# Kernel optimization log

Measured on AMD Instinct MI355X. Metric: run time of the kernel, lower is better.

The kernel has to match this reference:

```python
import jax, jax.numpy as jnp
import numpy as np

# LIF neuron constants (the CUDA kernel source is not shipped; these are the
# standard fused SNN semantics documented for this layer)
V_DECAY = 0.9       # membrane leak per step
V_THRESH = 1.0      # spike threshold
REFRAC_PERIOD = 5.0 # refractory timer reset value (in steps)

B_SZ, SEQ, HID, STATE = 8, 4096, 1024, 64


def setup_inputs() -> dict:
    key = jax.random.key(0)
    k1, k2, k3, k4, k5 = jax.random.split(key, 5)
    return {
        "input": jax.random.normal(k1, (B_SZ, SEQ, HID), dtype=jnp.float32),
        "ssm_A": jax.random.normal(k2, (STATE, STATE), dtype=jnp.float32) * 0.01,
        "ssm_B": jax.random.normal(k3, (STATE, 1), dtype=jnp.float32) * 0.1,
        "ssm_C": jax.random.normal(k4, (1, STATE), dtype=jnp.float32) * 0.1,
        "ssm_D": jax.random.normal(k5, (1, 1), dtype=jnp.float32) * 0.01,
    }


def reference(input, ssm_A, ssm_B, ssm_C, ssm_D):
    batch, seq_len, hidden = input.shape
    state = ssm_A.shape[0]

    # initial states (module.forward always starts from zeros)
    v0 = jnp.zeros((batch, hidden), dtype=jnp.float32)
    r0 = jnp.zeros((batch, hidden), dtype=jnp.float32)
    h0 = jnp.zeros((batch, state), dtype=jnp.float32)

    Bvec = ssm_B[:, 0]      # [state]
    Cvec = ssm_C[0, :]      # [state]
    Dsc = ssm_D[0, 0]       # scalar

    def step(carry, x_t):
        v, r, h = carry
        # --- SNN membrane + refractory update ---
        v = v * V_DECAY + x_t
        active = r <= 0.0
        spike = jnp.where(active & (v >= V_THRESH), 1.0, 0.0)  # [B,H]
        v = jnp.where(spike > 0.0, 0.0, v)
        r = jnp.where(spike > 0.0, REFRAC_PERIOD, jnp.maximum(r - 1.0, 0.0))
        # --- SSM recurrence, driven by pooled spike rate (scalar per batch) ---
        u = jnp.mean(spike, axis=-1)                 # [B]
        h = jnp.einsum('ns,bs->bn', ssm_A, h) + u[:, None] * Bvec  # [B,N]
        y = h @ Cvec + Dsc * u                       # [B]
        out_t = spike + y[:, None]                   # [B,H]
        return (v, r, h), out_t

    xs = jnp.swapaxes(input, 0, 1)                   # [S,B,H]
    _, ys = jax.lax.scan(step, (v0, r0, h0), xs)
    return jnp.swapaxes(ys, 0, 1)                    # [B,S,H]
```

## Files before the change

### kernel.cpp

```cpp
#include <hip/hip_runtime.h>
#include <cstdint>
#include <cstddef>

#define B_SZ   8
#define SEQ    4096
#define HID    1024
#define NCH    8
#define CHUNK  512
#define WARM   256
#define JTAP   16
#define TS     32

typedef float vfloat4 __attribute__((ext_vector_type(4)));

__device__ __forceinline__ void snn_step(float& v, float& r, float xv, bool& s) {
  v = __fadd_rn(__fmul_rn(v, 0.9f), xv);
  s = (r <= 0.0f) && (v >= 1.0f);
  v = s ? 0.0f : v;
  r = s ? 5.0f : fmaxf(r - 1.0f, 0.0f);
}

__device__ __forceinline__ void proc32_emit(const float* xv, float& v, float& r, int lane,
                                            unsigned long long* __restrict__ sp, int t) {
  unsigned long long my = 0;
  #pragma unroll
  for (int k = 0; k < 32; ++k) {
    bool s; snn_step(v, r, xv[k], s);
    unsigned long long m = __ballot(s);
    my = ((lane & 31) == k) ? m : my;
  }
  if (lane < 32) sp[t + lane] = my;
}

__device__ __forceinline__ void proc32_warm(const float* xv, float& v, float& r) {
  #pragma unroll
  for (int k = 0; k < 32; ++k) { bool s; snn_step(v, r, xv[k], s); }
}

__global__ __launch_bounds__(256) void snn_kernel(const float* __restrict__ x,
                                                  unsigned long long* __restrict__ spk) {
  const int hid  = blockIdx.x * 256 + threadIdx.x;
  const int b    = blockIdx.y;
  const int c    = blockIdx.z;
  const int lane = threadIdx.x & 63;
  const int wv   = hid >> 6;
  const int t0   = c * CHUNK;
  const int t1   = t0 + CHUNK;
  const int tw   = (t0 >= WARM) ? (t0 - WARM) : 0;
  const float* __restrict__ xp = x + (size_t)(b * SEQ) * HID + hid;
  unsigned long long* __restrict__ sp = spk + (size_t)(b * 16 + wv) * SEQ;

  float v = 0.0f, r = 0.0f;
  float xa[32], xb[32];

  #pragma unroll
  for (int k = 0; k < 32; ++k) xa[k] = xp[(size_t)(tw + k) * HID];

  for (int t = tw; t < t1; t += 64) {
    #pragma unroll
    for (int k = 0; k < 32; ++k) xb[k] = xp[(size_t)(t + 32 + k) * HID];

    if (t >= t0) proc32_emit(xa, v, r, lane, sp, t);
    else         proc32_warm(xa, v, r);

    if (t + 64 < t1) {
      #pragma unroll
      for (int k = 0; k < 32; ++k) xa[k] = xp[(size_t)(t + 64 + k) * HID];
    }

    if (t + 32 >= t0) proc32_emit(xb, v, r, lane, sp, t + 32);
    else              proc32_warm(xb, v, r);
  }
}

__global__ __launch_bounds__(256) void yout_kernel(const unsigned long long* __restrict__ spk,
                                                   const float* __restrict__ A,
                                                   const float* __restrict__ Bv,
                                                   const float* __restrict__ Cv,
                                                   const float* __restrict__ Dp,
                                                   vfloat4* __restrict__ out) {
  __shared__ unsigned long long lm[16][TS + JTAP];
  __shared__ float ws[JTAP];
  __shared__ float su[TS + JTAP];
  __shared__ float sy[TS];

  const int tid = threadIdx.x;
  const int b   = blockIdx.y;
  const int t0  = blockIdx.x * TS;
  const unsigned long long* __restrict__ sb = spk + (size_t)b * 16 * SEQ;

  if (tid < 64) {
    const int lane = tid;
    float arow[64];
    #pragma unroll 8
    for (int s2 = 0; s2 < 64; ++s2) arow[s2] = A[lane * 64 + s2];
    float p = Bv[lane];
    const float cv = Cv[lane];
    for (int m = 0; m < JTAP; ++m) {
      float t = cv * p;
      #pragma unroll
      for (int off = 32; off; off >>= 1) t += __shfl_xor(t, off);
      if (lane == 0) ws[m] = t;
      float n0 = 0.f, n1 = 0.f, n2 = 0.f, n3 = 0.f;
      #pragma unroll
      for (int s2 = 0; s2 < 64; s2 += 4) {
        n0 = fmaf(arow[s2 + 0], __shfl(p, s2 + 0), n0);
        n1 = fmaf(arow[s2 + 1], __shfl(p, s2 + 1), n1);
        n2 = fmaf(arow[s2 + 2], __shfl(p, s2 + 2), n2);
        n3 = fmaf(arow[s2 + 3], __shfl(p, s2 + 3), n3);
      }
      p = (n0 + n1) + (n2 + n3);
    }
  } else {
    const int i = tid - 64;
    if (i < TS + JTAP) {
      const int t = t0 - JTAP + i;
      #pragma unroll
      for (int wv = 0; wv < 16; ++wv)
        lm[wv][i] = (t >= 0) ? sb[(size_t)wv * SEQ + t] : 0ull;
    }
  }
  __syncthreads();

  if (tid < TS + JTAP) {
    int cc = 0;
    #pragma unroll
    for (int wv = 0; wv < 16; ++wv) cc += __popcll(lm[wv][tid]);
    su[tid] = cc * (1.0f / 1024.0f);
  }
  __syncthreads();

  if (tid < TS) {
    float acc = Dp[0] * su[JTAP + tid];
    #pragma unroll
    for (int m = 0; m < JTAP; ++m) acc = fmaf(ws[m], su[JTAP + tid - m], acc);
    sy[tid] = acc;
  }
  __syncthreads();

  const int wv = tid >> 4;
  const int sh = (tid & 15) * 4;
  vfloat4* op = out + (size_t)(b * SEQ + t0) * 256 + tid;
  #pragma unroll 8
  for (int j = 0; j < TS; ++j) {
    const unsigned long long m = lm[wv][JTAP + j];
    const float yv = sy[j];
    vfloat4 o;
    o.x = ((m >> (sh + 0)) & 1ull) ? 1.0f + yv : yv;
    o.y = ((m >> (sh + 1)) & 1ull) ? 1.0f + yv : yv;
    o.z = ((m >> (sh + 2)) & 1ull) ? 1.0f + yv : yv;
    o.w = ((m >> (sh + 3)) & 1ull) ? 1.0f + yv : yv;
    __builtin_nontemporal_store(o, &op[(size_t)j * 256]);
  }
}

extern "C" void kernel_launch(void* const* d_in, const int* in_sizes, int n_in,
                              void* d_out, int out_size, void* d_ws, size_t ws_size,
                              hipStream_t stream) {
  const float* x  = (const float*)d_in[0];
  const float* A  = (const float*)d_in[1];
  const float* Bv = (const float*)d_in[2];
  const float* Cv = (const float*)d_in[3];
  const float* Dp = (const float*)d_in[4];

  unsigned long long* spk = (unsigned long long*)d_ws;

  dim3 g1(HID / 256, B_SZ, NCH);
  snn_kernel<<<g1, 256, 0, stream>>>(x, spk);

  dim3 g2(SEQ / TS, B_SZ);
  yout_kernel<<<g2, 256, 0, stream>>>(spk, A, Bv, Cv, Dp, (vfloat4*)d_out);
}
```

Baseline: 284.1 us.

## Split y computation from output write and double SNN chunk parallelism

Halves the SNN chunk length (16 chunks of 256 steps with a 256-step warmup), doubling grid parallelism at the cost of more redundant warmup work. The combined y/output kernel is split in two. A new ssm_y kernel computes the pooled spike rate and the 16-tap y filter for 256 timesteps per block, so the 64-lane A-power setup is amortized over far more timesteps, and writes y to a workspace buffer. A separate out kernel then streams the output tiles with small 16-timestep blocks, adding one extra launch and a small y round trip through global memory.

```diff
diff --git a/kernel.cpp b/kernel.cpp
--- a/kernel.cpp
+++ b/kernel.cpp
@@ -5,11 +5,12 @@
 #define B_SZ   8
 #define SEQ    4096
 #define HID    1024
-#define NCH    8
-#define CHUNK  512
+#define NCH    16
+#define CHUNK  256
 #define WARM   256
 #define JTAP   16
-#define TS     32
+#define TS3    16
+#define YTS    256
 
 typedef float vfloat4 __attribute__((ext_vector_type(4)));
 
@@ -73,20 +74,18 @@
   }
 }
 
-__global__ __launch_bounds__(256) void yout_kernel(const unsigned long long* __restrict__ spk,
-                                                   const float* __restrict__ A,
-                                                   const float* __restrict__ Bv,
-                                                   const float* __restrict__ Cv,
-                                                   const float* __restrict__ Dp,
-                                                   vfloat4* __restrict__ out) {
-  __shared__ unsigned long long lm[16][TS + JTAP];
+__global__ __launch_bounds__(256) void ssm_y_kernel(const unsigned long long* __restrict__ spk,
+                                                    const float* __restrict__ A,
+                                                    const float* __restrict__ Bv,
+                                                    const float* __restrict__ Cv,
+                                                    const float* __restrict__ Dp,
+                                                    float* __restrict__ y) {
   __shared__ float ws[JTAP];
-  __shared__ float su[TS + JTAP];
-  __shared__ float sy[TS];
+  __shared__ float su[YTS + JTAP];
 
   const int tid = threadIdx.x;
   const int b   = blockIdx.y;
-  const int t0  = blockIdx.x * TS;
+  const int t0  = blockIdx.x * YTS;
   const unsigned long long* __restrict__ sb = spk + (size_t)b * 16 * SEQ;
 
   if (tid < 64) {
@@ -113,37 +112,47 @@
     }
   } else {
     const int i = tid - 64;
-    if (i < TS + JTAP) {
-      const int t = t0 - JTAP + i;
+    for (int j = i; j < YTS + JTAP; j += 192) {
+      const int t = t0 - JTAP + j;
+      int cc = 0;
       #pragma unroll
       for (int wv = 0; wv < 16; ++wv)
-        lm[wv][i] = (t >= 0) ? sb[(size_t)wv * SEQ + t] : 0ull;
+        cc += (t >= 0) ? __popcll(sb[(size_t)wv * SEQ + t]) : 0;
+      su[j] = cc * (1.0f / 1024.0f);
     }
   }
   __syncthreads();
 
-  if (tid < TS + JTAP) {
-    int cc = 0;
+  {
+    const int j = tid;
+    float acc = Dp[0] * su[JTAP + j];
     #pragma unroll
-    for (int wv = 0; wv < 16; ++wv) cc += __popcll(lm[wv][tid]);
-    su[tid] = cc * (1.0f / 1024.0f);
+    for (int m = 0; m < JTAP; ++m) acc = fmaf(ws[m], su[JTAP + j - m], acc);
+    y[(size_t)b * SEQ + t0 + j] = acc;
   }
-  __syncthreads();
+}
 
-  if (tid < TS) {
-    float acc = Dp[0] * su[JTAP + tid];
-    #pragma unroll
-    for (int m = 0; m < JTAP; ++m) acc = fmaf(ws[m], su[JTAP + tid - m], acc);
-    sy[tid] = acc;
-  }
+__global__ __launch_bounds__(256) void out_kernel(const unsigned long long* __restrict__ spk,
+                                                  const float* __restrict__ y,
+                                                  vfloat4* __restrict__ out) {
+  __shared__ unsigned long long lm[16][TS3 + 1];
+  __shared__ float sy[TS3];
+
+  const int tid = threadIdx.x;
+  const int b   = blockIdx.y;
+  const int t0  = blockIdx.x * TS3;
+  const unsigned long long* __restrict__ sb = spk + (size_t)b * 16 * SEQ;
+
+  lm[tid >> 4][tid & 15] = sb[(size_t)(tid >> 4) * SEQ + t0 + (tid & 15)];
+  if (tid < TS3) sy[tid] = y[(size_t)b * SEQ + t0 + tid];
   __syncthreads();
 
   const int wv = tid >> 4;
   const int sh = (tid & 15) * 4;
   vfloat4* op = out + (size_t)(b * SEQ + t0) * 256 + tid;
-  #pragma unroll 8
-  for (int j = 0; j < TS; ++j) {
-    const unsigned long long m = lm[wv][JTAP + j];
+  #pragma unroll
+  for (int j = 0; j < TS3; ++j) {
+    const unsigned long long m = lm[wv][j];
     const float yv = sy[j];
     vfloat4 o;
     o.x = ((m >> (sh + 0)) & 1ull) ? 1.0f + yv : yv;
@@ -164,10 +173,14 @@
   const float* Dp = (const float*)d_in[4];
 
   unsigned long long* spk = (unsigned long long*)d_ws;
+  float* yv = (float*)((char*)d_ws + ((size_t)B_SZ * 16 * SEQ * 8));
 
   dim3 g1(HID / 256, B_SZ, NCH);
   snn_kernel<<<g1, 256, 0, stream>>>(x, spk);
 
-  dim3 g2(SEQ / TS, B_SZ);
-  yout_kernel<<<g2, 256, 0, stream>>>(spk, A, Bv, Cv, Dp, (vfloat4*)d_out);
+  dim3 g2(SEQ / YTS, B_SZ);
+  ssm_y_kernel<<<g2, 256, 0, stream>>>(spk, A, Bv, Cv, Dp, yv);
+
+  dim3 g3(SEQ / TS3, B_SZ);
+  out_kernel<<<g3, 256, 0, stream>>>(spk, yv, (vfloat4*)d_out);
 }
```

Measured after the change: 287.1 us. No clear change (+1.1%).

## Fuse SNN scan and output kernels into one cooperative kernel with grid sync

Applied to the files above, without the earlier changes.

Merges the spike-generation kernel and the SSM/output kernel into a single cooperative launch of 256 blocks, separated by a grid-wide barrier, which removes one kernel launch and the gap between the two kernels. The output phase now handles 128 timesteps per block instead of 32, and the shared spike-mask tile is transposed and padded to spread the load work across threads. The nontemporal output store is replaced by a plain store. The costs are the grid-sync overhead and larger per-block output tiles, and the design relies on all 256 blocks being co-resident.

```diff
diff --git a/kernel.cpp b/kernel.cpp
--- a/kernel.cpp
+++ b/kernel.cpp
@@ -1,6 +1,9 @@
 #include <hip/hip_runtime.h>
+#include <hip/hip_cooperative_groups.h>
 #include <cstdint>
 #include <cstddef>
+
+namespace cg = cooperative_groups;
 
 #define B_SZ   8
 #define SEQ    4096
@@ -9,7 +12,7 @@
 #define CHUNK  512
 #define WARM   256
 #define JTAP   16
-#define TS     32
+#define YTS    128
 
 typedef float vfloat4 __attribute__((ext_vector_type(4)));
 
@@ -37,57 +40,64 @@
   for (int k = 0; k < 32; ++k) { bool s; snn_step(v, r, xv[k], s); }
 }
 
-__global__ __launch_bounds__(256) void snn_kernel(const float* __restrict__ x,
-                                                  unsigned long long* __restrict__ spk) {
-  const int hid  = blockIdx.x * 256 + threadIdx.x;
-  const int b    = blockIdx.y;
-  const int c    = blockIdx.z;
-  const int lane = threadIdx.x & 63;
-  const int wv   = hid >> 6;
-  const int t0   = c * CHUNK;
-  const int t1   = t0 + CHUNK;
-  const int tw   = (t0 >= WARM) ? (t0 - WARM) : 0;
-  const float* __restrict__ xp = x + (size_t)(b * SEQ) * HID + hid;
-  unsigned long long* __restrict__ sp = spk + (size_t)(b * 16 + wv) * SEQ;
-
-  float v = 0.0f, r = 0.0f;
-  float xa[32], xb[32];
-
-  #pragma unroll
-  for (int k = 0; k < 32; ++k) xa[k] = xp[(size_t)(tw + k) * HID];
-
-  for (int t = tw; t < t1; t += 64) {
-    #pragma unroll
-    for (int k = 0; k < 32; ++k) xb[k] = xp[(size_t)(t + 32 + k) * HID];
-
-    if (t >= t0) proc32_emit(xa, v, r, lane, sp, t);
-    else         proc32_warm(xa, v, r);
-
-    if (t + 64 < t1) {
-      #pragma unroll
-      for (int k = 0; k < 32; ++k) xa[k] = xp[(size_t)(t + 64 + k) * HID];
-    }
-
-    if (t + 32 >= t0) proc32_emit(xb, v, r, lane, sp, t + 32);
-    else              proc32_warm(xb, v, r);
-  }
-}
-
-__global__ __launch_bounds__(256) void yout_kernel(const unsigned long long* __restrict__ spk,
-                                                   const float* __restrict__ A,
-                                                   const float* __restrict__ Bv,
-                                                   const float* __restrict__ Cv,
-                                                   const float* __restrict__ Dp,
-                                                   vfloat4* __restrict__ out) {
-  __shared__ unsigned long long lm[16][TS + JTAP];
+__global__ __launch_bounds__(256) void fused_kernel(const float* __restrict__ x,
+                                                    const float* __restrict__ A,
+                                                    const float* __restrict__ Bv,
+                                                    const float* __restrict__ Cv,
+                                                    const float* __restrict__ Dp,
+                                                    unsigned long long* __restrict__ spk,
+                                                    vfloat4* __restrict__ out) {
+  __shared__ unsigned long long lm[YTS + JTAP][17];
   __shared__ float ws[JTAP];
-  __shared__ float su[TS + JTAP];
-  __shared__ float sy[TS];
+  __shared__ float su[YTS + JTAP];
+  __shared__ float sy[YTS];
 
   const int tid = threadIdx.x;
-  const int b   = blockIdx.y;
-  const int t0  = blockIdx.x * TS;
-  const unsigned long long* __restrict__ sb = spk + (size_t)b * 16 * SEQ;
+  const int bi  = blockIdx.x;
+
+  {
+    const int hidq = bi & 3;
+    const int b    = (bi >> 2) & 7;
+    const int c    = bi >> 5;
+    const int hid  = hidq * 256 + tid;
+    const int lane = tid & 63;
+    const int wv   = hid >> 6;
+    const int t0   = c * CHUNK;
+    const int t1   = t0 + CHUNK;
+    const int tw   = (t0 >= WARM) ? (t0 - WARM) : 0;
+    const float* __restrict__ xp = x + (size_t)(b * SEQ) * HID + hid;
+    unsigned long long* __restrict__ sp = spk + (size_t)(b * 16 + wv) * SEQ;
+
+    float v = 0.0f, r = 0.0f;
+    float xa[32], xb[32];
+
+    #pragma unroll
+    for (int k = 0; k < 32; ++k) xa[k] = xp[(size_t)(tw + k) * HID];
+
+    for (int t = tw; t < t1; t += 64) {
+      #pragma unroll
+      for (int k = 0; k < 32; ++k) xb[k] = xp[(size_t)(t + 32 + k) * HID];
+
+      if (t >= t0) proc32_emit(xa, v, r, lane, sp, t);
+      else         proc32_warm(xa, v, r);
+
+      if (t + 64 < t1) {
+        #pragma unroll
+        for (int k = 0; k < 32; ++k) xa[k] = xp[(size_t)(t + 64 + k) * HID];
+      }
+
+      if (t + 32 >= t0) proc32_emit(xb, v, r, lane, sp, t + 32);
+      else              proc32_warm(xb, v, r);
+    }
+  }
+
+  __threadfence();
+  cg::this_grid().sync();
+  __threadfence();
+
+  const int b2 = bi >> 5;
+  const int t0 = (bi & 31) * YTS;
+  const unsigned long long* __restrict__ sb = spk + (size_t)b2 * 16 * SEQ;
 
   if (tid < 64) {
     const int lane = tid;
@@ -112,25 +122,27 @@
       p = (n0 + n1) + (n2 + n3);
     }
   } else {
-    const int i = tid - 64;
-    if (i < TS + JTAP) {
+    const int j  = tid - 64;
+    const int wv = j & 15;
+    const int i0 = (j >> 4) * 12;
+    #pragma unroll
+    for (int s = 0; s < 12; ++s) {
+      const int i = i0 + s;
       const int t = t0 - JTAP + i;
-      #pragma unroll
-      for (int wv = 0; wv < 16; ++wv)
-        lm[wv][i] = (t >= 0) ? sb[(size_t)wv * SEQ + t] : 0ull;
+      lm[i][wv] = (t >= 0) ? sb[(size_t)wv * SEQ + t] : 0ull;
     }
   }
   __syncthreads();
 
-  if (tid < TS + JTAP) {
+  if (tid < YTS + JTAP) {
     int cc = 0;
     #pragma unroll
-    for (int wv = 0; wv < 16; ++wv) cc += __popcll(lm[wv][tid]);
+    for (int wv = 0; wv < 16; ++wv) cc += __popcll(lm[tid][wv]);
     su[tid] = cc * (1.0f / 1024.0f);
   }
   __syncthreads();
 
-  if (tid < TS) {
+  if (tid < YTS) {
     float acc = Dp[0] * su[JTAP + tid];
     #pragma unroll
     for (int m = 0; m < JTAP; ++m) acc = fmaf(ws[m], su[JTAP + tid - m], acc);
@@ -140,17 +152,17 @@
 
   const int wv = tid >> 4;
   const int sh = (tid & 15) * 4;
-  vfloat4* op = out + (size_t)(b * SEQ + t0) * 256 + tid;
+  vfloat4* op = out + (size_t)(b2 * SEQ + t0) * 256 + tid;
   #pragma unroll 8
-  for (int j = 0; j < TS; ++j) {
-    const unsigned long long m = lm[wv][JTAP + j];
+  for (int j = 0; j < YTS; ++j) {
+    const unsigned long long m = lm[JTAP + j][wv];
     const float yv = sy[j];
     vfloat4 o;
     o.x = ((m >> (sh + 0)) & 1ull) ? 1.0f + yv : yv;
     o.y = ((m >> (sh + 1)) & 1ull) ? 1.0f + yv : yv;
     o.z = ((m >> (sh + 2)) & 1ull) ? 1.0f + yv : yv;
     o.w = ((m >> (sh + 3)) & 1ull) ? 1.0f + yv : yv;
-    __builtin_nontemporal_store(o, &op[(size_t)j * 256]);
+    op[(size_t)j * 256] = o;
   }
 }
 
@@ -164,10 +176,10 @@
   const float* Dp = (const float*)d_in[4];
 
   unsigned long long* spk = (unsigned long long*)d_ws;
+  vfloat4* outp = (vfloat4*)d_out;
 
-  dim3 g1(HID / 256, B_SZ, NCH);
-  snn_kernel<<<g1, 256, 0, stream>>>(x, spk);
-
-  dim3 g2(SEQ / TS, B_SZ);
-  yout_kernel<<<g2, 256, 0, stream>>>(spk, A, Bv, Cv, Dp, (vfloat4*)d_out);
+  void* args[] = {(void*)&x, (void*)&A, (void*)&Bv, (void*)&Cv, (void*)&Dp,
+                  (void*)&spk, (void*)&outp};
+  hipLaunchCooperativeKernel((const void*)fused_kernel, dim3(256), dim3(256),
+                             args, 0, stream);
 }
```

After: 346.7 us. 22.0% more time.
